# Performance work log

Hardware: AMD Instinct MI355X
Metric: run time of the kernel (lower is better)

## Reference

```python
import jax, jax.numpy as jnp
import numpy as np

B, S, A, H = 32, 256, 6, 1024
OBS, GLOB, MASK, AGF = 520, 30, 52, 73
NTYPE = 5


def setup_inputs() -> dict:
    key = jax.random.key(0)
    ks = jax.random.split(key, 24)
    inputs = jax.random.normal(ks[0], (B, S, OBS), dtype=jnp.float32)
    # per-agent player-type lives at concat-column 1 -> raw column 30 + a*73 + 1
    types = jax.random.randint(ks[1], (B, A), 0, NTYPE).astype(jnp.float32)
    cols = np.array(GLOB + np.arange(A) * AGF + 1)
    inputs = inputs.at[:, :, cols].set(jnp.broadcast_to(types[:, None, :], (B, S, A)))
    # binary action mask in the last 52 columns
    mask = jax.random.bernoulli(ks[2], 0.7, (B, S, MASK)).astype(jnp.float32)
    inputs = inputs.at[:, :, -MASK:].set(mask)
    sc = 0.05
    p = {
        'inputs': inputs,
        'state0': jnp.zeros((B, A * H), dtype=jnp.float32),
        'W_emb': jax.random.normal(ks[3], (NTYPE, 102, 512)) * sc,
        'b_emb': jax.random.normal(ks[4], (NTYPE, 512)) * sc,
        'W_ih': jax.random.normal(ks[5], (3 * H, 512)) * sc,
        'W_hh': jax.random.normal(ks[6], (3 * H, H)) * sc,
        'b_ih': jax.random.normal(ks[7], (3 * H,)) * sc,
        'b_hh': jax.random.normal(ks[8], (3 * H,)) * sc,
        'Wg0': jax.random.normal(ks[9], (H, 4, 256)) * sc,
        'a0s': jax.random.normal(ks[10], (4, 256)) * sc,
        'a0d': jax.random.normal(ks[11], (4, 256)) * sc,
        'Wg1': jax.random.normal(ks[12], (H, 4, 256)) * sc,
        'a1s': jax.random.normal(ks[13], (4, 256)) * sc,
        'a1d': jax.random.normal(ks[14], (4, 256)) * sc,
        'Wa1': jax.random.normal(ks[15], (NTYPE, H, 512)) * sc,
        'ba1': jax.random.normal(ks[16], (NTYPE, 512)) * sc,
        'Wa2': jax.random.normal(ks[17], (NTYPE, 512, 52)) * sc,
        'ba2': jax.random.normal(ks[18], (NTYPE, 52)) * sc,
    }
    return p


def _gat(x, W, a_s, a_d):
    # x: [B, N, F]; standard multi-head GAT over the fully-connected agent graph
    hf = jnp.einsum('bnf,fhd->bnhd', x, W)
    src = jnp.einsum('bnhd,hd->bhn', hf, a_s)
    dst = jnp.einsum('bnhd,hd->bhn', hf, a_d)
    e = jax.nn.leaky_relu(src[:, :, :, None] + dst[:, :, None, :], 0.2)  # [b,h,i,j]
    att = jax.nn.softmax(e, axis=-1)
    out = jnp.einsum('bhij,bjhd->bihd', att, hf)
    return jax.nn.elu(out.reshape(x.shape[0], x.shape[1], -1))


def reference(inputs, state0, W_emb, b_emb, W_ih, W_hh, b_ih, b_hh,
              Wg0, a0s, a0d, Wg1, a1s, a1d, Wa1, ba1, Wa2, ba2):
    b, s, _ = inputs.shape
    masks = inputs[:, :, -MASK:]
    glob = inputs[:, :, :GLOB]
    agent = inputs[:, :, GLOB:-MASK].reshape(b, s, A, AGF)
    x = jnp.concatenate([agent, jnp.broadcast_to(glob[:, :, None, :], (b, s, A, GLOB))], -1)
    x = x.transpose(0, 2, 1, 3).reshape(b * A, s, AGF + GLOB)  # [N, S, 103]
    vec = x[:, :, 1:]                                           # [N, S, 102]
    types = vec[:, 0, 0].astype(jnp.int32)                      # per-agent player type
    # type-routed Linear + ReLU (grouped GEMM instead of the python loop)
    emb = jax.nn.relu(jnp.einsum('nsf,nfd->nsd', vec, W_emb[types]) + b_emb[types][:, None, :])
    # single-layer GRU, batched over all B*A agents
    xg = emb @ W_ih.T + b_ih                                    # [N, S, 3H]
    h0 = state0.reshape(b * A, H)

    def step(h, xt):
        hg = h @ W_hh.T + b_hh
        xr, xz, xn = jnp.split(xt, 3, axis=-1)
        hr, hz, hn = jnp.split(hg, 3, axis=-1)
        r = jax.nn.sigmoid(xr + hr)
        z = jax.nn.sigmoid(xz + hz)
        n = jnp.tanh(xn + r * hn)
        return (1.0 - z) * n + z * h, None

    hT, _ = jax.lax.scan(step, h0, xg.transpose(1, 0, 2))       # final hidden == last output
    g0 = _gat(hT.reshape(b, A, H), Wg0, a0s, a0d)
    g1 = _gat(g0, Wg1, a1s, a1d)
    f0 = g1[:, 0, :]                                            # agent-0 features [B, 1024]
    pt = types.reshape(b, A)[:, 0]                              # per-sample routing type
    h1 = jax.nn.relu(jnp.einsum('bf,bfd->bd', f0, Wa1[pt]) + ba1[pt])
    logits = jnp.einsum('bf,bfd->bd', h1, Wa2[pt]) + ba2[pt]    # [B, 52]
    logits = logits[:, None, :]                                 # [B, 1, 52]
    action_logit = jnp.where(masks != 0, logits, jnp.zeros_like(logits))  # broadcast -> [B, S, 52]
    return action_logit, hT
```

## Files before the change

### kernel.cpp

```cpp
#include <hip/hip_runtime.h>
#include <hip/hip_bf16.h>
#include <cmath>

#define BB    32
#define SS    256
#define AA    6
#define HH    1024
#define OBSF  520
#define GLOBF 30
#define MASKF 52
#define AGFF  73
#define NSEQ  192
#define EMBD  512

#define GRID_GRU 256
#define THR_GRU  192
#define LDS_W_BYTES (48*3*64*16)

typedef short bf16x8 __attribute__((ext_vector_type(8)));
typedef float f32x4  __attribute__((ext_vector_type(4)));

__device__ __forceinline__ float sigmoidf_(float x){ return 1.f/(1.f + expf(-x)); }
__device__ __forceinline__ short f2bf(float x){
    __hip_bfloat16 h = __float2bfloat16(x);
    return *reinterpret_cast<short*>(&h);
}

__device__ __forceinline__ bf16x8 load_bypass16(const short* p){
    union { unsigned long long u[2]; bf16x8 v; } x;
    x.u[0] = __hip_atomic_load((const unsigned long long*)p,     __ATOMIC_RELAXED, __HIP_MEMORY_SCOPE_AGENT);
    x.u[1] = __hip_atomic_load((const unsigned long long*)(p+4), __ATOMIC_RELAXED, __HIP_MEMORY_SCOPE_AGENT);
    return x.v;
}

__device__ __forceinline__ void mg_barrier(unsigned* cnt, unsigned target)
{
    asm volatile("s_waitcnt vmcnt(0)" ::: "memory");
    __syncthreads();
    if (threadIdx.x == 0) {
        __hip_atomic_fetch_add(cnt, 1u, __ATOMIC_RELAXED, __HIP_MEMORY_SCOPE_AGENT);
        while (__hip_atomic_load(cnt, __ATOMIC_RELAXED, __HIP_MEMORY_SCOPE_AGENT) < target)
            __builtin_amdgcn_s_sleep(1);
    }
    __syncthreads();
}

__global__ __launch_bounds__(256) void cvt_bf16(
    const float* __restrict__ in, __hip_bfloat16* __restrict__ out, int n)
{
    for (int i = blockIdx.x*256 + threadIdx.x; i < n; i += gridDim.x*256)
        out[i] = __float2bfloat16(in[i]);
}

__global__ __launch_bounds__(256) void emb_kernel(
    const float* __restrict__ inp, const float* __restrict__ W_emb,
    const float* __restrict__ b_emb, __hip_bfloat16* __restrict__ emb)
{
    const int n  = blockIdx.x;
    const int s0 = blockIdx.y * 16;
    const int b  = n / AA, a = n % AA;
    const int tid = threadIdx.x;
    const int ty = (int)inp[(size_t)(b*SS)*OBSF + GLOBF + a*AGFF + 1];

    __shared__ float vecs[16][102];
    for (int idx = tid; idx < 16*102; idx += 256) {
        int ss = idx / 102, f = idx % 102;
        int g  = f + 1;
        int col = (g < AGFF) ? (GLOBF + a*AGFF + g) : (g - AGFF);
        vecs[ss][f] = inp[((size_t)(b*SS + s0 + ss))*OBSF + col];
    }
    __syncthreads();

    float acc0[16], acc1[16];
    #pragma unroll
    for (int ss = 0; ss < 16; ++ss) { acc0[ss] = 0.f; acc1[ss] = 0.f; }

    const float* Wb = W_emb + (size_t)ty*102*EMBD;
    for (int f = 0; f < 102; ++f) {
        float w0 = Wb[f*EMBD + tid];
        float w1 = Wb[f*EMBD + tid + 256];
        #pragma unroll
        for (int ss = 0; ss < 16; ++ss) {
            float v = vecs[ss][f];
            acc0[ss] += v * w0;
            acc1[ss] += v * w1;
        }
    }
    float bb0 = b_emb[ty*EMBD + tid], bb1 = b_emb[ty*EMBD + tid + 256];
    for (int ss = 0; ss < 16; ++ss) {
        __hip_bfloat16* o = emb + ((size_t)n*SS + s0 + ss)*EMBD;
        o[tid]       = __float2bfloat16(fmaxf(acc0[ss] + bb0, 0.f));
        o[tid + 256] = __float2bfloat16(fmaxf(acc1[ss] + bb1, 0.f));
    }
}

__global__ __launch_bounds__(THR_GRU, 1) void gru_persistent(
    const float* __restrict__ state0,
    const short* __restrict__ emb_bf,
    const short* __restrict__ Whh_bf, const short* __restrict__ Wih_bf,
    const float* __restrict__ b_ih, const float* __restrict__ b_hh,
    short* __restrict__ hbf0, short* __restrict__ hbf1,
    float* __restrict__ hT_out, unsigned* __restrict__ bar)
{
    extern __shared__ short ldsW[];
    __shared__ short ldsH[3*256];
    const int tid = threadIdx.x, wave = tid >> 6, lane = tid & 63;
    const int nt = blockIdx.x & 63, mg = blockIdx.x >> 6;
    const int i0 = nt*16, mt = mg*3 + wave;
    const int col = lane & 15, rgrp = lane >> 4;
    const int n = i0 + col;
    unsigned* cnt = bar + mg*32;

    for (int idx = tid; idx < 32*3*64; idx += THR_GRU) {
        int l = idx & 63, g = (idx >> 6) % 3, kt = idx / 192;
        const short* src = Whh_bf + ((size_t)(g*HH + i0 + (l & 15)))*HH + kt*32 + (l >> 4)*8;
        *(bf16x8*)(ldsW + (size_t)idx*8) = *(const bf16x8*)src;
    }
    short* ldsW2 = ldsW + 32*3*64*8;
    for (int idx = tid; idx < 16*3*64; idx += THR_GRU) {
        int l = idx & 63, g = (idx >> 6) % 3, kt = idx / 192;
        const short* src = Wih_bf + ((size_t)(g*HH + i0 + (l & 15)))*EMBD + kt*32 + (l >> 4)*8;
        *(bf16x8*)(ldsW2 + (size_t)idx*8) = *(const bf16x8*)src;
    }

    float hreg[4];
    #pragma unroll
    for (int r_ = 0; r_ < 4; ++r_) {
        hreg[r_] = state0[(size_t)(mt*16 + rgrp*4 + r_)*HH + n];
        ldsH[wave*256 + (rgrp*4 + r_)*16 + col] = f2bf(hreg[r_]);
    }
    __syncthreads();
    {
        int w2 = tid >> 6, rem = tid & 63, rr = rem >> 2, cg = rem & 3;
        unsigned long long v = *(const unsigned long long*)(ldsH + w2*256 + rr*16 + cg*4);
        __hip_atomic_store((unsigned long long*)(hbf0 + (size_t)((mg*3 + w2)*16 + rr)*HH + i0 + cg*4),
                           v, __ATOMIC_RELAXED, __HIP_MEMORY_SCOPE_AGENT);
    }
    const float bir = b_ih[n], biz = b_ih[HH+n], bin_ = b_ih[2*HH+n];
    const float bhr = b_hh[n], bhz = b_hh[HH+n], bhn  = b_hh[2*HH+n];

    const size_t lane_h_off = (size_t)(mt*16 + col)*HH + rgrp*8;
    const size_t lane_e_off = (size_t)(mt*16 + col)*SS*EMBD + rgrp*8;

    mg_barrier(cnt, 64);

    for (int s = 0; s < SS; ++s) {
        const short* cur = (s & 1) ? hbf1 : hbf0;
        short*       nxt = (s & 1) ? hbf0 : hbf1;
        f32x4 a0 = {0.f,0.f,0.f,0.f}, a1 = a0, a2 = a0, a3 = a0;

        const short* Ah = cur + lane_h_off;
        bf16x8 fa[2][8];
        #pragma unroll
        for (int j = 0; j < 8; ++j) fa[0][j] = load_bypass16(Ah + j*32);
        #pragma unroll
        for (int g = 0; g < 4; ++g) {
            if (g < 3) {
                #pragma unroll
                for (int j = 0; j < 8; ++j)
                    fa[(g+1)&1][j] = load_bypass16(Ah + ((g+1)*8 + j)*32);
            }
            #pragma unroll
            for (int j = 0; j < 8; ++j) {
                const int kt = g*8 + j;
                bf16x8 b0 = *(const bf16x8*)(ldsW + ((kt*3 + 0)*64 + lane)*8);
                bf16x8 b1 = *(const bf16x8*)(ldsW + ((kt*3 + 1)*64 + lane)*8);
                bf16x8 b2 = *(const bf16x8*)(ldsW + ((kt*3 + 2)*64 + lane)*8);
                a0 = __builtin_amdgcn_mfma_f32_16x16x32_bf16(fa[g&1][j], b0, a0, 0,0,0);
                a1 = __builtin_amdgcn_mfma_f32_16x16x32_bf16(fa[g&1][j], b1, a1, 0,0,0);
                a2 = __builtin_amdgcn_mfma_f32_16x16x32_bf16(fa[g&1][j], b2, a2, 0,0,0);
            }
        }
        const short* Ae = emb_bf + lane_e_off + (size_t)s*EMBD;
        #pragma unroll 8
        for (int kt = 0; kt < 16; ++kt) {
            bf16x8 a  = *(const bf16x8*)(Ae + kt*32);
            bf16x8 b0 = *(const bf16x8*)(ldsW2 + ((kt*3 + 0)*64 + lane)*8);
            bf16x8 b1 = *(const bf16x8*)(ldsW2 + ((kt*3 + 1)*64 + lane)*8);
            bf16x8 b2 = *(const bf16x8*)(ldsW2 + ((kt*3 + 2)*64 + lane)*8);
            a0 = __builtin_amdgcn_mfma_f32_16x16x32_bf16(a, b0, a0, 0,0,0);
            a1 = __builtin_amdgcn_mfma_f32_16x16x32_bf16(a, b1, a1, 0,0,0);
            a3 = __builtin_amdgcn_mfma_f32_16x16x32_bf16(a, b2, a3, 0,0,0);
        }
        #pragma unroll
        for (int r_ = 0; r_ < 4; ++r_) {
            float r  = sigmoidf_(a0[r_] + bir + bhr);
            float z  = sigmoidf_(a1[r_] + biz + bhz);
            float nn = tanhf(a3[r_] + bin_ + r*(a2[r_] + bhn));
            float hv = (1.f - z)*nn + z*hreg[r_];
            hreg[r_] = hv;
            ldsH[wave*256 + (rgrp*4 + r_)*16 + col] = f2bf(hv);
        }
        __syncthreads();
        {
            int w2 = tid >> 6, rem = tid & 63, rr = rem >> 2, cg = rem & 3;
            unsigned long long v = *(const unsigned long long*)(ldsH + w2*256 + rr*16 + cg*4);
            __hip_atomic_store((unsigned long long*)(nxt + (size_t)((mg*3 + w2)*16 + rr)*HH + i0 + cg*4),
                               v, __ATOMIC_RELAXED, __HIP_MEMORY_SCOPE_AGENT);
        }
        mg_barrier(cnt, 64u*(unsigned)(s + 2));
    }

    #pragma unroll
    for (int r_ = 0; r_ < 4; ++r_)
        hT_out[(size_t)(mt*16 + rgrp*4 + r_)*HH + n] = hreg[r_];
}

__global__ __launch_bounds__(256) void gru_step_mfma(
    const float* __restrict__ h_in, const __hip_bfloat16* __restrict__ h_in_bf,
    float* __restrict__ h_out, __hip_bfloat16* __restrict__ h_out_bf,
    const __hip_bfloat16* __restrict__ emb_bf,
    const __hip_bfloat16* __restrict__ Whh_bf, const __hip_bfloat16* __restrict__ Wih_bf,
    const float* __restrict__ b_ih, const float* __restrict__ b_hh, int s)
{
    const int i0   = blockIdx.x * 16;
    const int tid  = threadIdx.x;
    const int wave = tid >> 6, lane = tid & 63;
    const int col  = lane & 15, rgrp = lane >> 4;
    const int n    = i0 + col;
    const int kofs = rgrp * 8;

    f32x4 acc[3][4];
    #pragma unroll
    for (int mi = 0; mi < 3; ++mi)
        #pragma unroll
        for (int g = 0; g < 4; ++g) acc[mi][g] = (f32x4){0.f,0.f,0.f,0.f};

    {
        const short* Ab = (const short*)h_in_bf;
        const short* B0 = (const short*)Whh_bf + ((size_t)(      n))*HH + kofs;
        const short* B1 = (const short*)Whh_bf + ((size_t)(HH  + n))*HH + kofs;
        const short* B2 = (const short*)Whh_bf + ((size_t)(2*HH+ n))*HH + kofs;
        #pragma unroll 2
        for (int kt = 0; kt < 32; ++kt) {
            const int kk = kt * 32;
            bf16x8 b0 = *(const bf16x8*)(B0 + kk);
            bf16x8 b1 = *(const bf16x8*)(B1 + kk);
            bf16x8 b2 = *(const bf16x8*)(B2 + kk);
            #pragma unroll
            for (int mi = 0; mi < 3; ++mi) {
                const int m = (wave*3 + mi)*16 + col;
                bf16x8 a = *(const bf16x8*)(Ab + (size_t)m*HH + kk + kofs);
                acc[mi][0] = __builtin_amdgcn_mfma_f32_16x16x32_bf16(a, b0, acc[mi][0], 0,0,0);
                acc[mi][1] = __builtin_amdgcn_mfma_f32_16x16x32_bf16(a, b1, acc[mi][1], 0,0,0);
                acc[mi][2] = __builtin_amdgcn_mfma_f32_16x16x32_bf16(a, b2, acc[mi][2], 0,0,0);
            }
        }
    }
    {
        const short* Ab = (const short*)emb_bf;
        const short* B0 = (const short*)Wih_bf + ((size_t)(      n))*EMBD + kofs;
        const short* B1 = (const short*)Wih_bf + ((size_t)(HH  + n))*EMBD + kofs;
        const short* B2 = (const short*)Wih_bf + ((size_t)(2*HH+ n))*EMBD + kofs;
        #pragma unroll 2
        for (int kt = 0; kt < 16; ++kt) {
            const int kk = kt * 32;
            bf16x8 b0 = *(const bf16x8*)(B0 + kk);
            bf16x8 b1 = *(const bf16x8*)(B1 + kk);
            bf16x8 b2 = *(const bf16x8*)(B2 + kk);
            #pragma unroll
            for (int mi = 0; mi < 3; ++mi) {
                const int m = (wave*3 + mi)*16 + col;
                bf16x8 a = *(const bf16x8*)(Ab + ((size_t)m*SS + s)*EMBD + kk + kofs);
                acc[mi][0] = __builtin_amdgcn_mfma_f32_16x16x32_bf16(a, b0, acc[mi][0], 0,0,0);
                acc[mi][1] = __builtin_amdgcn_mfma_f32_16x16x32_bf16(a, b1, acc[mi][1], 0,0,0);
                acc[mi][3] = __builtin_amdgcn_mfma_f32_16x16x32_bf16(a, b2, acc[mi][3], 0,0,0);
            }
        }
    }
    const float bir = b_ih[n], biz = b_ih[HH + n], bin_ = b_ih[2*HH + n];
    const float bhr = b_hh[n], bhz = b_hh[HH + n], bhn  = b_hh[2*HH + n];
    #pragma unroll
    for (int mi = 0; mi < 3; ++mi) {
        #pragma unroll
        for (int r_ = 0; r_ < 4; ++r_) {
            const int m = (wave*3 + mi)*16 + rgrp*4 + r_;
            float r  = sigmoidf_(acc[mi][0][r_] + bir + bhr);
            float z  = sigmoidf_(acc[mi][1][r_] + biz + bhz);
            float nn = tanhf(acc[mi][3][r_] + bin_ + r*(acc[mi][2][r_] + bhn));
            const size_t idx = (size_t)m*HH + n;
            float hv = (1.f - z)*nn + z*h_in[idx];
            h_out[idx]    = hv;
            h_out_bf[idx] = __float2bfloat16(hv);
        }
    }
}

__global__ __launch_bounds__(256) void sgemm_rrr(
    const float* __restrict__ A, const float* __restrict__ B,
    float* __restrict__ C, int M, int N, int K)
{
    const int n0 = blockIdx.x * 64;
    const int m0 = blockIdx.y * 64;
    const int tid = threadIdx.x;
    const int tn = tid & 15, tm = tid >> 4;

    __shared__ float As[16][68];
    __shared__ float Bs[16][68];
    float acc[4][4];
    #pragma unroll
    for (int i = 0; i < 4; ++i)
        #pragma unroll
        for (int j = 0; j < 4; ++j) acc[i][j] = 0.f;

    for (int k0 = 0; k0 < K; k0 += 16) {
        {
            int ml = tid >> 2, k4 = (tid & 3) << 2;
            float4 av = *(const float4*)(A + (size_t)(m0 + ml)*K + k0 + k4);
            As[k4 + 0][ml] = av.x; As[k4 + 1][ml] = av.y;
            As[k4 + 2][ml] = av.z; As[k4 + 3][ml] = av.w;
            int kl = tid >> 4, n4 = (tid & 15) << 2;
            *(float4*)&Bs[kl][n4] = *(const float4*)(B + (size_t)(k0 + kl)*N + n0 + n4);
        }
        __syncthreads();
        #pragma unroll
        for (int kk = 0; kk < 16; ++kk) {
            float4 a4 = *(float4*)&As[kk][tm << 2];
            float4 b4 = *(float4*)&Bs[kk][tn << 2];
            acc[0][0] += a4.x*b4.x; acc[0][1] += a4.x*b4.y; acc[0][2] += a4.x*b4.z; acc[0][3] += a4.x*b4.w;
            acc[1][0] += a4.y*b4.x; acc[1][1] += a4.y*b4.y; acc[1][2] += a4.y*b4.z; acc[1][3] += a4.y*b4.w;
            acc[2][0] += a4.z*b4.x; acc[2][1] += a4.z*b4.y; acc[2][2] += a4.z*b4.z; acc[2][3] += a4.z*b4.w;
            acc[3][0] += a4.w*b4.x; acc[3][1] += a4.w*b4.y; acc[3][2] += a4.w*b4.z; acc[3][3] += a4.w*b4.w;
        }
        __syncthreads();
    }
    #pragma unroll
    for (int qm = 0; qm < 4; ++qm) {
        float4 v = make_float4(acc[qm][0], acc[qm][1], acc[qm][2], acc[qm][3]);
        *(float4*)(C + (size_t)(m0 + tm*4 + qm)*N + n0 + tn*4) = v;
    }
}

__global__ __launch_bounds__(256) void gat_att(
    const float* __restrict__ hf, const float* __restrict__ a_s,
    const float* __restrict__ a_d, float* __restrict__ gout)
{
    const int b = blockIdx.x;
    const int tid = threadIdx.x;
    __shared__ float hfs[6][1024];
    __shared__ float srcs[24], dsts[24];
    __shared__ float att[4][36];

    for (int idx = tid; idx < 6*1024; idx += 256)
        hfs[idx >> 10][idx & 1023] = hf[(size_t)b*6144 + idx];
    __syncthreads();

    const int w = tid >> 6, lane = tid & 63;
    for (int p = w; p < 24; p += 4) {
        int h = p / 6, nn = p % 6;
        float as_ = 0.f, ad_ = 0.f;
        for (int c = lane; c < 256; c += 64) {
            float v = hfs[nn][h*256 + c];
            as_ += v * a_s[h*256 + c];
            ad_ += v * a_d[h*256 + c];
        }
        #pragma unroll
        for (int off = 32; off; off >>= 1) {
            as_ += __shfl_down(as_, off);
            ad_ += __shfl_down(ad_, off);
        }
        if (lane == 0) { srcs[p] = as_; dsts[p] = ad_; }
    }
    __syncthreads();

    if (tid < 24) {
        int h = tid / 6, i = tid % 6;
        float e[6], mx = -1e30f;
        #pragma unroll
        for (int j = 0; j < 6; ++j) {
            float x = srcs[h*6 + i] + dsts[h*6 + j];
            e[j] = (x >= 0.f) ? x : 0.2f*x;
            mx = fmaxf(mx, e[j]);
        }
        float sum = 0.f;
        #pragma unroll
        for (int j = 0; j < 6; ++j) { e[j] = expf(e[j] - mx); sum += e[j]; }
        float inv = 1.f / sum;
        #pragma unroll
        for (int j = 0; j < 6; ++j) att[h][i*6 + j] = e[j]*inv;
    }
    __syncthreads();

    for (int idx = tid; idx < 6144; idx += 256) {
        int i = idx >> 10, hd = idx & 1023, h = hd >> 8;
        float v = 0.f;
        #pragma unroll
        for (int j = 0; j < 6; ++j) v += att[h][i*6 + j] * hfs[j][hd];
        gout[(size_t)b*6144 + idx] = (v > 0.f) ? v : (expf(v) - 1.f);
    }
}

__global__ __launch_bounds__(256) void head_kernel(
    const float* __restrict__ g1, const float* __restrict__ inp,
    const float* __restrict__ Wa1, const float* __restrict__ ba1,
    const float* __restrict__ Wa2, const float* __restrict__ ba2,
    float* __restrict__ out)
{
    const int b = blockIdx.x;
    const int tid = threadIdx.x;
    const int pt = (int)inp[(size_t)b*SS*OBSF + GLOBF + 1];

    __shared__ float f0s[1024];
    __shared__ float h1s[512];
    __shared__ float lgs[52];

    for (int idx = tid; idx < 1024; idx += 256) f0s[idx] = g1[(size_t)b*6144 + idx];
    __syncthreads();
    {
        float acc0 = 0.f, acc1 = 0.f;
        const float* W = Wa1 + (size_t)pt*1024*512;
        for (int f = 0; f < 1024; ++f) {
            float v = f0s[f];
            acc0 += v * W[f*512 + tid];
            acc1 += v * W[f*512 + tid + 256];
        }
        h1s[tid]       = fmaxf(acc0 + ba1[pt*512 + tid], 0.f);
        h1s[tid + 256] = fmaxf(acc1 + ba1[pt*512 + tid + 256], 0.f);
    }
    __syncthreads();
    if (tid < 52) {
        float acc = 0.f;
        const float* W = Wa2 + (size_t)pt*512*52;
        for (int f = 0; f < 512; ++f) acc += h1s[f] * W[f*52 + tid];
        lgs[tid] = acc + ba2[pt*52 + tid];
    }
    __syncthreads();
    for (int idx = tid; idx < SS*MASKF; idx += 256) {
        int s = idx / MASKF, c = idx % MASKF;
        float mv = inp[((size_t)b*SS + s)*OBSF + (OBSF - MASKF) + c];
        out[(size_t)b*SS*MASKF + idx] = (mv != 0.f) ? lgs[c] : 0.f;
    }
}

extern "C" void kernel_launch(void* const* d_in, const int* in_sizes, int n_in,
                              void* d_out, int out_size, void* d_ws, size_t ws_size,
                              hipStream_t stream)
{
    const float* inp    = (const float*)d_in[0];
    const float* state0 = (const float*)d_in[1];
    const float* W_emb  = (const float*)d_in[2];
    const float* b_emb  = (const float*)d_in[3];
    const float* W_ih   = (const float*)d_in[4];
    const float* W_hh   = (const float*)d_in[5];
    const float* b_ih   = (const float*)d_in[6];
    const float* b_hh   = (const float*)d_in[7];
    const float* Wg0    = (const float*)d_in[8];
    const float* a0s    = (const float*)d_in[9];
    const float* a0d    = (const float*)d_in[10];
    const float* Wg1    = (const float*)d_in[11];
    const float* a1s    = (const float*)d_in[12];
    const float* a1d    = (const float*)d_in[13];
    const float* Wa1    = (const float*)d_in[14];
    const float* ba1    = (const float*)d_in[15];
    const float* Wa2    = (const float*)d_in[16];
    const float* ba2    = (const float*)d_in[17];
    float* out = (float*)d_out;

    char* p = (char*)d_ws;
    __hip_bfloat16* emb_bf = (__hip_bfloat16*)p;  p += (size_t)NSEQ*SS*EMBD*2;
    __hip_bfloat16* Whh_bf = (__hip_bfloat16*)p;  p += (size_t)3*HH*HH*2;
    __hip_bfloat16* Wih_bf = (__hip_bfloat16*)p;  p += (size_t)3*HH*EMBD*2;
    float* hb0 = (float*)p;                       p += (size_t)NSEQ*HH*4;
    float* hb1 = (float*)p;                       p += (size_t)NSEQ*HH*4;
    short* hbf0 = (short*)p;                      p += (size_t)NSEQ*HH*2;
    short* hbf1 = (short*)p;                      p += (size_t)NSEQ*HH*2;
    float* hf = (float*)p;                        p += (size_t)NSEQ*HH*4;
    float* g0 = (float*)p;                        p += (size_t)NSEQ*HH*4;
    float* g1 = (float*)p;                        p += (size_t)NSEQ*HH*4;
    unsigned* bar = (unsigned*)p;                 p += 512;
    if (ws_size < (size_t)(p - (char*)d_ws)) return;

    cvt_bf16<<<512, 256, 0, stream>>>(W_hh, Whh_bf, 3*HH*HH);
    cvt_bf16<<<512, 256, 0, stream>>>(W_ih, Wih_bf, 3*HH*EMBD);

    emb_kernel<<<dim3(NSEQ, 16), 256, 0, stream>>>(inp, W_emb, b_emb, emb_bf);

    hipMemsetAsync(bar, 0, 512, stream);
    float* hT_out = out + (size_t)BB*SS*MASKF;

    static int attr_set = 0;
    if (!attr_set) {
        hipFuncSetAttribute((const void*)gru_persistent,
                            hipFuncAttributeMaxDynamicSharedMemorySize, LDS_W_BYTES);
        attr_set = 1;
    }
    const short* emb_bf_s = (const short*)emb_bf;
    const short* Whh_bf_s = (const short*)Whh_bf;
    const short* Wih_bf_s = (const short*)Wih_bf;
    void* args[] = { (void*)&state0, (void*)&emb_bf_s, (void*)&Whh_bf_s, (void*)&Wih_bf_s,
                     (void*)&b_ih, (void*)&b_hh, (void*)&hbf0, (void*)&hbf1,
                     (void*)&hT_out, (void*)&bar };
    hipError_t e = hipLaunchCooperativeKernel((const void*)gru_persistent,
                                              dim3(GRID_GRU), dim3(THR_GRU),
                                              args, LDS_W_BYTES, stream);
    const float* hT;
    if (e == hipSuccess) {
        hT = hT_out;
    } else {
        cvt_bf16<<<192, 256, 0, stream>>>(state0, (__hip_bfloat16*)hbf0, NSEQ*HH);
        hipMemcpyAsync(hb0, state0, (size_t)NSEQ*HH*4, hipMemcpyDeviceToDevice, stream);
        float* hf32[2] = {hb0, hb1};
        short* hbf[2] = {hbf0, hbf1};
        for (int s = 0; s < SS; ++s) {
            gru_step_mfma<<<64, 256, 0, stream>>>(
                hf32[s & 1], (const __hip_bfloat16*)hbf[s & 1],
                hf32[(s + 1) & 1], (__hip_bfloat16*)hbf[(s + 1) & 1],
                (const __hip_bfloat16*)emb_bf, Whh_bf, Wih_bf, b_ih, b_hh, s);
        }
        hT = hb0;
        hipMemcpyAsync(hT_out, hb0, (size_t)NSEQ*HH*4, hipMemcpyDeviceToDevice, stream);
    }

    sgemm_rrr<<<dim3(16, 3), 256, 0, stream>>>(hT, Wg0, hf, NSEQ, HH, HH);
    gat_att<<<BB, 256, 0, stream>>>(hf, a0s, a0d, g0);
    sgemm_rrr<<<dim3(16, 3), 256, 0, stream>>>(g0, Wg1, hf, NSEQ, HH, HH);
    gat_att<<<BB, 256, 0, stream>>>(hf, a1s, a1d, g1);

    head_kernel<<<BB, 256, 0, stream>>>(g1, inp, Wa1, ba1, Wa2, ba2, out);
}
```

Before: 3.308 ms.

## Merge GRU blocks into 64 wide workgroups and overlap input projection with barrier wait

```diff
diff --git a/kernel.cpp b/kernel.cpp
--- a/kernel.cpp
+++ b/kernel.cpp
@@ -13,8 +13,8 @@
 #define NSEQ  192
 #define EMBD  512
 
-#define GRID_GRU 256
-#define THR_GRU  192
+#define GRID_GRU 64
+#define THR_GRU  768
 #define LDS_W_BYTES (48*3*64*16)
 
 typedef short bf16x8 __attribute__((ext_vector_type(8)));
@@ -31,18 +31,6 @@
     x.u[0] = __hip_atomic_load((const unsigned long long*)p,     __ATOMIC_RELAXED, __HIP_MEMORY_SCOPE_AGENT);
     x.u[1] = __hip_atomic_load((const unsigned long long*)(p+4), __ATOMIC_RELAXED, __HIP_MEMORY_SCOPE_AGENT);
     return x.v;
-}
-
-__device__ __forceinline__ void mg_barrier(unsigned* cnt, unsigned target)
-{
-    asm volatile("s_waitcnt vmcnt(0)" ::: "memory");
-    __syncthreads();
-    if (threadIdx.x == 0) {
-        __hip_atomic_fetch_add(cnt, 1u, __ATOMIC_RELAXED, __HIP_MEMORY_SCOPE_AGENT);
-        while (__hip_atomic_load(cnt, __ATOMIC_RELAXED, __HIP_MEMORY_SCOPE_AGENT) < target)
-            __builtin_amdgcn_s_sleep(1);
-    }
-    __syncthreads();
 }
 
 __global__ __launch_bounds__(256) void cvt_bf16(
@@ -94,7 +82,7 @@
     }
 }
 
-__global__ __launch_bounds__(THR_GRU, 1) void gru_persistent(
+__global__ __launch_bounds__(THR_GRU, 3) void gru_persistent(
     const float* __restrict__ state0,
     const short* __restrict__ emb_bf,
     const short* __restrict__ Whh_bf, const short* __restrict__ Wih_bf,
@@ -103,13 +91,13 @@
     float* __restrict__ hT_out, unsigned* __restrict__ bar)
 {
     extern __shared__ short ldsW[];
-    __shared__ short ldsH[3*256];
+    __shared__ short ldsH[12*256];
     const int tid = threadIdx.x, wave = tid >> 6, lane = tid & 63;
-    const int nt = blockIdx.x & 63, mg = blockIdx.x >> 6;
-    const int i0 = nt*16, mt = mg*3 + wave;
+    const int nt = blockIdx.x;
+    const int i0 = nt*16, mt = wave;
     const int col = lane & 15, rgrp = lane >> 4;
     const int n = i0 + col;
-    unsigned* cnt = bar + mg*32;
+    unsigned* cnt = bar;
 
     for (int idx = tid; idx < 32*3*64; idx += THR_GRU) {
         int l = idx & 63, g = (idx >> 6) % 3, kt = idx / 192;
@@ -133,21 +121,44 @@
     {
         int w2 = tid >> 6, rem = tid & 63, rr = rem >> 2, cg = rem & 3;
         unsigned long long v = *(const unsigned long long*)(ldsH + w2*256 + rr*16 + cg*4);
-        __hip_atomic_store((unsigned long long*)(hbf0 + (size_t)((mg*3 + w2)*16 + rr)*HH + i0 + cg*4),
+        __hip_atomic_store((unsigned long long*)(hbf0 + (size_t)(w2*16 + rr)*HH + i0 + cg*4),
                            v, __ATOMIC_RELAXED, __HIP_MEMORY_SCOPE_AGENT);
     }
+    asm volatile("s_waitcnt vmcnt(0)" ::: "memory");
+    __syncthreads();
+    if (tid == 0)
+        __hip_atomic_fetch_add(cnt, 1u, __ATOMIC_RELAXED, __HIP_MEMORY_SCOPE_AGENT);
+
     const float bir = b_ih[n], biz = b_ih[HH+n], bin_ = b_ih[2*HH+n];
     const float bhr = b_hh[n], bhz = b_hh[HH+n], bhn  = b_hh[2*HH+n];
 
     const size_t lane_h_off = (size_t)(mt*16 + col)*HH + rgrp*8;
     const size_t lane_e_off = (size_t)(mt*16 + col)*SS*EMBD + rgrp*8;
 
-    mg_barrier(cnt, 64);
+    f32x4 ax0 = {0.f,0.f,0.f,0.f}, ax1 = ax0, ax3 = ax0;
+    {
+        const short* Ae = emb_bf + lane_e_off;
+        #pragma unroll 8
+        for (int kt = 0; kt < 16; ++kt) {
+            bf16x8 a  = *(const bf16x8*)(Ae + kt*32);
+            bf16x8 b0 = *(const bf16x8*)(ldsW2 + ((kt*3 + 0)*64 + lane)*8);
+            bf16x8 b1 = *(const bf16x8*)(ldsW2 + ((kt*3 + 1)*64 + lane)*8);
+            bf16x8 b2 = *(const bf16x8*)(ldsW2 + ((kt*3 + 2)*64 + lane)*8);
+            ax0 = __builtin_amdgcn_mfma_f32_16x16x32_bf16(a, b0, ax0, 0,0,0);
+            ax1 = __builtin_amdgcn_mfma_f32_16x16x32_bf16(a, b1, ax1, 0,0,0);
+            ax3 = __builtin_amdgcn_mfma_f32_16x16x32_bf16(a, b2, ax3, 0,0,0);
+        }
+    }
+    if (tid == 0) {
+        while (__hip_atomic_load(cnt, __ATOMIC_RELAXED, __HIP_MEMORY_SCOPE_AGENT) < 64u)
+            __builtin_amdgcn_s_sleep(1);
+    }
+    __syncthreads();
 
     for (int s = 0; s < SS; ++s) {
         const short* cur = (s & 1) ? hbf1 : hbf0;
         short*       nxt = (s & 1) ? hbf0 : hbf1;
-        f32x4 a0 = {0.f,0.f,0.f,0.f}, a1 = a0, a2 = a0, a3 = a0;
+        f32x4 a0 = {0.f,0.f,0.f,0.f}, a1 = a0, a2 = a0;
 
         const short* Ah = cur + lane_h_off;
         bf16x8 fa[2][8];
@@ -171,22 +182,11 @@
                 a2 = __builtin_amdgcn_mfma_f32_16x16x32_bf16(fa[g&1][j], b2, a2, 0,0,0);
             }
         }
-        const short* Ae = emb_bf + lane_e_off + (size_t)s*EMBD;
-        #pragma unroll 8
-        for (int kt = 0; kt < 16; ++kt) {
-            bf16x8 a  = *(const bf16x8*)(Ae + kt*32);
-            bf16x8 b0 = *(const bf16x8*)(ldsW2 + ((kt*3 + 0)*64 + lane)*8);
-            bf16x8 b1 = *(const bf16x8*)(ldsW2 + ((kt*3 + 1)*64 + lane)*8);
-            bf16x8 b2 = *(const bf16x8*)(ldsW2 + ((kt*3 + 2)*64 + lane)*8);
-            a0 = __builtin_amdgcn_mfma_f32_16x16x32_bf16(a, b0, a0, 0,0,0);
-            a1 = __builtin_amdgcn_mfma_f32_16x16x32_bf16(a, b1, a1, 0,0,0);
-            a3 = __builtin_amdgcn_mfma_f32_16x16x32_bf16(a, b2, a3, 0,0,0);
-        }
         #pragma unroll
         for (int r_ = 0; r_ < 4; ++r_) {
-            float r  = sigmoidf_(a0[r_] + bir + bhr);
-            float z  = sigmoidf_(a1[r_] + biz + bhz);
-            float nn = tanhf(a3[r_] + bin_ + r*(a2[r_] + bhn));
+            float r  = sigmoidf_(ax0[r_] + a0[r_] + bir + bhr);
+            float z  = sigmoidf_(ax1[r_] + a1[r_] + biz + bhz);
+            float nn = tanhf(ax3[r_] + bin_ + r*(a2[r_] + bhn));
             float hv = (1.f - z)*nn + z*hreg[r_];
             hreg[r_] = hv;
             ldsH[wave*256 + (rgrp*4 + r_)*16 + col] = f2bf(hv);
@@ -195,10 +195,34 @@
         {
             int w2 = tid >> 6, rem = tid & 63, rr = rem >> 2, cg = rem & 3;
             unsigned long long v = *(const unsigned long long*)(ldsH + w2*256 + rr*16 + cg*4);
-            __hip_atomic_store((unsigned long long*)(nxt + (size_t)((mg*3 + w2)*16 + rr)*HH + i0 + cg*4),
+            __hip_atomic_store((unsigned long long*)(nxt + (size_t)(w2*16 + rr)*HH + i0 + cg*4),
                                v, __ATOMIC_RELAXED, __HIP_MEMORY_SCOPE_AGENT);
         }
-        mg_barrier(cnt, 64u*(unsigned)(s + 2));
+        asm volatile("s_waitcnt vmcnt(0)" ::: "memory");
+        __syncthreads();
+        if (tid == 0)
+            __hip_atomic_fetch_add(cnt, 1u, __ATOMIC_RELAXED, __HIP_MEMORY_SCOPE_AGENT);
+
+        if (s < SS-1) {
+            ax0 = (f32x4){0.f,0.f,0.f,0.f}; ax1 = ax0; ax3 = ax0;
+            const short* Ae = emb_bf + lane_e_off + (size_t)(s+1)*EMBD;
+            #pragma unroll 8
+            for (int kt = 0; kt < 16; ++kt) {
+                bf16x8 a  = *(const bf16x8*)(Ae + kt*32);
+                bf16x8 b0 = *(const bf16x8*)(ldsW2 + ((kt*3 + 0)*64 + lane)*8);
+                bf16x8 b1 = *(const bf16x8*)(ldsW2 + ((kt*3 + 1)*64 + lane)*8);
+                bf16x8 b2 = *(const bf16x8*)(ldsW2 + ((kt*3 + 2)*64 + lane)*8);
+                ax0 = __builtin_amdgcn_mfma_f32_16x16x32_bf16(a, b0, ax0, 0,0,0);
+                ax1 = __builtin_amdgcn_mfma_f32_16x16x32_bf16(a, b1, ax1, 0,0,0);
+                ax3 = __builtin_amdgcn_mfma_f32_16x16x32_bf16(a, b2, ax3, 0,0,0);
+            }
+            if (tid == 0) {
+                unsigned target = 64u*(unsigned)(s + 2);
+                while (__hip_atomic_load(cnt, __ATOMIC_RELAXED, __HIP_MEMORY_SCOPE_AGENT) < target)
+                    __builtin_amdgcn_s_sleep(1);
+            }
+            __syncthreads();
+        }
     }
 
     #pragma unroll
```

Result: slower. 7.758 ms (+134.5%).
